# Optimization experiments

Measured on AMD Instinct MI355X. Metric: run time of the kernel, lower is better.

## Reference

```python
import jax, jax.numpy as jnp
import numpy as np

D_MODEL = 512
NHEAD = 8
WINDOW = 32  # attends to [i-32, i+32]


def setup_inputs() -> dict:
    key = jax.random.key(0)
    ks = jax.random.split(key, 5)
    B, S, D = 2, 2048, D_MODEL
    return {
        "x": jax.random.normal(ks[0], (B, S, D), dtype=jnp.float32),
        "w_qkv": jax.random.normal(ks[1], (D, 3 * D), dtype=jnp.float32) * 0.02,
        "b_qkv": jax.random.normal(ks[2], (3 * D,), dtype=jnp.float32) * 0.02,
        "w_out": jax.random.normal(ks[3], (D, D), dtype=jnp.float32) * 0.02,
        "b_out": jax.random.normal(ks[4], (D,), dtype=jnp.float32) * 0.02,
    }


def reference(x, w_qkv, b_qkv, w_out, b_out):
    B, S, D = x.shape
    H = NHEAD
    hd = D // H
    w = WINDOW
    W = 2 * w + 1

    qkv = (x @ w_qkv + b_qkv).reshape(B, S, 3, H, hd)
    q, k, v = qkv[:, :, 0], qkv[:, :, 1], qkv[:, :, 2]  # [B,S,H,hd]

    # window indices per query position: [S, W]
    idx = jnp.arange(S)[:, None] + jnp.arange(-w, w + 1)[None, :]
    valid = (idx >= 0) & (idx < S)
    idx_c = jnp.clip(idx, 0, S - 1)

    k_win = k[:, idx_c]  # [B,S,W,H,hd]
    v_win = v[:, idx_c]  # [B,S,W,H,hd]

    scale = 1.0 / (hd ** 0.5)
    scores = jnp.einsum('bshd,bswhd->bshw', q, k_win) * scale  # [B,S,H,W]
    scores = jnp.where(valid[None, :, None, :], scores, -1e9)
    attn = jax.nn.softmax(scores, axis=-1)
    out = jnp.einsum('bshw,bswhd->bshd', attn, v_win).reshape(B, S, D)
    return out @ w_out + b_out
```

## Files before the change

kernel.cpp:

```cpp
#include <hip/hip_runtime.h>


typedef __bf16 bf16x8 __attribute__((ext_vector_type(8)));
typedef float  f32x4  __attribute__((ext_vector_type(4)));
typedef unsigned short u16;
typedef unsigned int   u32;

__device__ __forceinline__ u16 f2bf(float f) {
  u32 u = __builtin_bit_cast(u32, f);
  u += 0x7FFFu + ((u >> 16) & 1u);
  return (u16)(u >> 16);
}
__device__ __forceinline__ u32 pack2(u16 a, u16 b) {
  return (u32)a | ((u32)b << 16);
}
__device__ __forceinline__ void glds16(const void* g, void* l) {
  __builtin_amdgcn_global_load_lds(
      (const __attribute__((address_space(1))) void*)g,
      (__attribute__((address_space(3))) void*)l, 16, 0, 0);
}
__device__ __forceinline__ f32x4 mfma16(bf16x8 a, bf16x8 b, f32x4 c) {
  return __builtin_amdgcn_mfma_f32_16x16x32_bf16(a, b, c, 0, 0, 0);
}

__global__ __launch_bounds__(256) void prep(
    const float4* __restrict__ X, uint2* __restrict__ XH,
    const float* __restrict__ Wq, u16* __restrict__ Wqt,
    const float* __restrict__ Wo, u16* __restrict__ Wot) {
  __shared__ float T[32][33];
  const int blk = blockIdx.x, t = threadIdx.x;
  if (blk < 2048) {
    int i = blk * 256 + t;
    float4 v = X[i];
    XH[i] = make_uint2(pack2(f2bf(v.x), f2bf(v.y)), pack2(f2bf(v.z), f2bf(v.w)));
    return;
  }
  const float* W;
  u16* Wt;
  int n0, k0, N;
  if (blk < 2816) {
    int idx = blk - 2048;
    W = Wq; Wt = Wqt; N = 1536;
    n0 = (idx % 48) * 32; k0 = (idx / 48) * 32;
  } else {
    int idx = blk - 2816;
    W = Wo; Wt = Wot; N = 512;
    n0 = (idx % 16) * 32; k0 = (idx / 16) * 32;
  }
  const int r = t >> 3, c = (t & 7) * 4;
  float4 v = *(const float4*)&W[(size_t)(k0 + r) * N + n0 + c];
  T[c][r] = v.x; T[c + 1][r] = v.y; T[c + 2][r] = v.z; T[c + 3][r] = v.w;
  __syncthreads();
  u16 a = f2bf(T[r][c]),      b = f2bf(T[r][c + 1]);
  u16 cc = f2bf(T[r][c + 2]), d = f2bf(T[r][c + 3]);
  *(uint2*)&Wt[(size_t)(n0 + r) * 512 + k0 + c] =
      make_uint2(pack2(a, b), pack2(cc, d));
}

__global__ __launch_bounds__(256) void gemm_qkv(
    const u16* __restrict__ Ah, const u16* __restrict__ Bt,
    const float* __restrict__ bias,
    u16* __restrict__ Qb, u16* __restrict__ Kb, u16* __restrict__ Vb) {
  __shared__ __align__(16) u16 sA[64 * 64];
  __shared__ __align__(16) u16 sB[128 * 64];

  const int t = threadIdx.x, l = t & 63, w = t >> 6;
  const int wm = w >> 1, wn = w & 1;
  const int mBase = blockIdx.y * 64, nBase = blockIdx.x * 128;

  const int rsub = l >> 3;
  const int qsrc = (l & 7) ^ (rsub & 7);
  const u16* gA0 = Ah + (size_t)(mBase + w * 16 + rsub) * 512 + qsrc * 8;
  const u16* gA1 = Ah + (size_t)(mBase + w * 16 + 8 + rsub) * 512 + qsrc * 8;
  u16* lA0 = sA + (w * 16) * 64;
  u16* lA1 = sA + (w * 16 + 8) * 64;
  const u16* gB[4];
  u16* lB[4];
#pragma unroll
  for (int j = 0; j < 4; ++j) {
    gB[j] = Bt + (size_t)(nBase + w * 32 + j * 8 + rsub) * 512 + qsrc * 8;
    lB[j] = sB + (w * 32 + j * 8) * 64;
  }

  const int r15 = l & 15, kg = l >> 4;
  const int sw = r15 & 7;
  int aoff[2][2], boff[4][2];
#pragma unroll
  for (int mt = 0; mt < 2; ++mt)
#pragma unroll
    for (int s = 0; s < 2; ++s)
      aoff[mt][s] = (wm * 32 + mt * 16 + r15) * 64 + (((s * 4 + kg) ^ sw) * 8);
#pragma unroll
  for (int nt = 0; nt < 4; ++nt)
#pragma unroll
    for (int s = 0; s < 2; ++s)
      boff[nt][s] = (wn * 64 + nt * 16 + r15) * 64 + (((s * 4 + kg) ^ sw) * 8);

  f32x4 acc[2][4];
#pragma unroll
  for (int i = 0; i < 2; ++i)
#pragma unroll
    for (int j = 0; j < 4; ++j) acc[i][j] = (f32x4){0.f, 0.f, 0.f, 0.f};

  for (int k0 = 0; k0 < 512; k0 += 64) {
    glds16(gA0 + k0, lA0);
    glds16(gA1 + k0, lA1);
#pragma unroll
    for (int j = 0; j < 4; ++j) glds16(gB[j] + k0, lB[j]);
    __syncthreads();
#pragma unroll
    for (int s = 0; s < 2; ++s) {
      bf16x8 b[4];
#pragma unroll
      for (int nt = 0; nt < 4; ++nt) b[nt] = *(const bf16x8*)(sB + boff[nt][s]);
      bf16x8 a0 = *(const bf16x8*)(sA + aoff[0][s]);
      bf16x8 a1 = *(const bf16x8*)(sA + aoff[1][s]);
#pragma unroll
      for (int nt = 0; nt < 4; ++nt) {
        acc[0][nt] = mfma16(a0, b[nt], acc[0][nt]);
        acc[1][nt] = mfma16(a1, b[nt], acc[1][nt]);
      }
    }
    __syncthreads();
  }

  const int lq = l >> 4;
  const int seg = nBase >> 9, colb = nBase & 511;
#pragma unroll
  for (int mt = 0; mt < 2; ++mt) {
    int row0 = mBase + wm * 32 + mt * 16 + lq * 4;
#pragma unroll
    for (int nt = 0; nt < 4; ++nt) {
      int col = wn * 64 + nt * 16 + r15;
      float bv = bias[nBase + col];
      int cc = colb + col;
      if (seg == 0) {
#pragma unroll
        for (int r = 0; r < 4; ++r)
          Qb[(size_t)(row0 + r) * 512 + cc] = f2bf((acc[mt][nt][r] + bv) * 0.125f);
      } else if (seg == 1) {
#pragma unroll
        for (int r = 0; r < 4; ++r)
          Kb[(size_t)(row0 + r) * 512 + cc] = f2bf(acc[mt][nt][r] + bv);
      } else {
#pragma unroll
        for (int r = 0; r < 4; ++r)
          Vb[(size_t)(row0 + r) * 512 + cc] = f2bf(acc[mt][nt][r] + bv);
      }
    }
  }
}

__global__ __launch_bounds__(256) void attn_mfma(
    const u16* __restrict__ Qb, const u16* __restrict__ Kb,
    const u16* __restrict__ Vb, u16* __restrict__ Oh) {
  const int tile = blockIdx.x, h = blockIdx.y, b = blockIdx.z;
  const int base = tile * 64;
  const size_t hb = (size_t)b * 2048;

  __shared__ __align__(16) u16 Qs[64][72];
  __shared__ __align__(16) u16 Ks[128][72];
  __shared__ __align__(16) u16 Vt[64][136];
  __shared__ __align__(16) u16 Pp[64][136];

  const int t = threadIdx.x, l = t & 63, w = t >> 6;
  const int r15 = l & 15, kg = l >> 4;

  {
    int r = t >> 2, c0 = (t & 3) * 16;
    const uint4* src = (const uint4*)&Qb[(hb + base + r) * 512 + h * 64 + c0];
    *(uint4*)&Qs[r][c0] = src[0];
    *(uint4*)&Qs[r][c0 + 8] = src[1];
  }
  {
    int j = t >> 1, half = (t & 1) * 32;
    int ja = min(max(base - 32 + j, 0), 2047);
    const uint4* src = (const uint4*)&Kb[(hb + ja) * 512 + h * 64 + half];
    uint4* dst = (uint4*)&Ks[j][half];
    dst[0] = src[0]; dst[1] = src[1]; dst[2] = src[2]; dst[3] = src[3];
  }
  {
    int j = t >> 1, ds = (t & 1) * 32;
    int ja = min(max(base - 32 + j, 0), 2047);
    const u16* src = &Vb[(hb + ja) * 512 + h * 64 + ds];
    u16 tmp[32];
    *(uint4*)&tmp[0]  = *(const uint4*)(src);
    *(uint4*)&tmp[8]  = *(const uint4*)(src + 8);
    *(uint4*)&tmp[16] = *(const uint4*)(src + 16);
    *(uint4*)&tmp[24] = *(const uint4*)(src + 24);
#pragma unroll
    for (int i = 0; i < 32; ++i) Vt[ds + i][j] = tmp[i];
  }
  __syncthreads();

  bf16x8 aQ0 = *(const bf16x8*)&Qs[w * 16 + r15][kg * 8];
  bf16x8 aQ1 = *(const bf16x8*)&Qs[w * 16 + r15][32 + kg * 8];
  f32x4 zero = (f32x4){0.f, 0.f, 0.f, 0.f};
  f32x4 sacc[8];
#pragma unroll
  for (int nt = 0; nt < 8; ++nt) {
    bf16x8 b0 = *(const bf16x8*)&Ks[nt * 16 + r15][kg * 8];
    bf16x8 b1 = *(const bf16x8*)&Ks[nt * 16 + r15][32 + kg * 8];
    sacc[nt] = mfma16(aQ0, b0, zero);
    sacc[nt] = mfma16(aQ1, b1, sacc[nt]);
  }

#pragma unroll
  for (int r = 0; r < 4; ++r) {
    int s_abs = base + w * 16 + kg * 4 + r;
    float m = -3.0e38f;
#pragma unroll
    for (int nt = 0; nt < 8; ++nt) {
      int j_abs = base - 32 + nt * 16 + r15;
      int dlt = j_abs - s_abs;
      bool valid = (dlt >= -32) && (dlt <= 32) && (j_abs >= 0) && (j_abs < 2048);
      float v = valid ? sacc[nt][r] : -1.0e9f;
      sacc[nt][r] = v;
      m = fmaxf(m, v);
    }
#pragma unroll
    for (int msk = 1; msk < 16; msk <<= 1) m = fmaxf(m, __shfl_xor(m, msk, 64));
    float s_ = 0.f;
#pragma unroll
    for (int nt = 0; nt < 8; ++nt) {
      float e = __expf(sacc[nt][r] - m);
      sacc[nt][r] = e;
      s_ += e;
    }
#pragma unroll
    for (int msk = 1; msk < 16; msk <<= 1) s_ += __shfl_xor(s_, msk, 64);
    float inv = 1.0f / s_;
#pragma unroll
    for (int nt = 0; nt < 8; ++nt)
      Pp[w * 16 + kg * 4 + r][nt * 16 + r15] = f2bf(sacc[nt][r] * inv);
  }
  __syncthreads();

  bf16x8 aP[4];
#pragma unroll
  for (int kt = 0; kt < 4; ++kt)
    aP[kt] = *(const bf16x8*)&Pp[w * 16 + r15][kt * 32 + kg * 8];
  f32x4 oacc[4];
#pragma unroll
  for (int nt = 0; nt < 4; ++nt) oacc[nt] = zero;
#pragma unroll
  for (int nt = 0; nt < 4; ++nt) {
#pragma unroll
    for (int kt = 0; kt < 4; ++kt) {
      bf16x8 bV = *(const bf16x8*)&Vt[nt * 16 + r15][kt * 32 + kg * 8];
      oacc[nt] = mfma16(aP[kt], bV, oacc[nt]);
    }
  }

#pragma unroll
  for (int nt = 0; nt < 4; ++nt) {
#pragma unroll
    for (int r = 0; r < 4; ++r) {
      size_t idx =
          (hb + base + w * 16 + kg * 4 + r) * 512 + h * 64 + nt * 16 + r15;
      Oh[idx] = f2bf(oacc[nt][r]);
    }
  }
}

__global__ __launch_bounds__(256) void gemm_out(
    const u16* __restrict__ Ah, const u16* __restrict__ Bt,
    const float* __restrict__ bias, float* __restrict__ Cf) {
  __shared__ __align__(16) u16 sA[64 * 64];
  __shared__ __align__(16) u16 sB[128 * 64];

  const int t = threadIdx.x, l = t & 63, w = t >> 6;
  const int wm = w >> 1, wn = w & 1;
  const int mBase = blockIdx.y * 64, nBase = blockIdx.x * 128;

  const int rsub = l >> 3;
  const int qsrc = (l & 7) ^ (rsub & 7);
  const u16* gA0 = Ah + (size_t)(mBase + w * 16 + rsub) * 512 + qsrc * 8;
  const u16* gA1 = Ah + (size_t)(mBase + w * 16 + 8 + rsub) * 512 + qsrc * 8;
  u16* lA0 = sA + (w * 16) * 64;
  u16* lA1 = sA + (w * 16 + 8) * 64;
  const u16* gB[4];
  u16* lB[4];
#pragma unroll
  for (int j = 0; j < 4; ++j) {
    gB[j] = Bt + (size_t)(nBase + w * 32 + j * 8 + rsub) * 512 + qsrc * 8;
    lB[j] = sB + (w * 32 + j * 8) * 64;
  }

  const int r15 = l & 15, kg = l >> 4;
  const int sw = r15 & 7;
  int aoff[2][2], boff[4][2];
#pragma unroll
  for (int mt = 0; mt < 2; ++mt)
#pragma unroll
    for (int s = 0; s < 2; ++s)
      aoff[mt][s] = (wm * 32 + mt * 16 + r15) * 64 + (((s * 4 + kg) ^ sw) * 8);
#pragma unroll
  for (int nt = 0; nt < 4; ++nt)
#pragma unroll
    for (int s = 0; s < 2; ++s)
      boff[nt][s] = (wn * 64 + nt * 16 + r15) * 64 + (((s * 4 + kg) ^ sw) * 8);

  f32x4 acc[2][4];
#pragma unroll
  for (int i = 0; i < 2; ++i)
#pragma unroll
    for (int j = 0; j < 4; ++j) acc[i][j] = (f32x4){0.f, 0.f, 0.f, 0.f};

  for (int k0 = 0; k0 < 512; k0 += 64) {
    glds16(gA0 + k0, lA0);
    glds16(gA1 + k0, lA1);
#pragma unroll
    for (int j = 0; j < 4; ++j) glds16(gB[j] + k0, lB[j]);
    __syncthreads();
#pragma unroll
    for (int s = 0; s < 2; ++s) {
      bf16x8 b[4];
#pragma unroll
      for (int nt = 0; nt < 4; ++nt) b[nt] = *(const bf16x8*)(sB + boff[nt][s]);
      bf16x8 a0 = *(const bf16x8*)(sA + aoff[0][s]);
      bf16x8 a1 = *(const bf16x8*)(sA + aoff[1][s]);
#pragma unroll
      for (int nt = 0; nt < 4; ++nt) {
        acc[0][nt] = mfma16(a0, b[nt], acc[0][nt]);
        acc[1][nt] = mfma16(a1, b[nt], acc[1][nt]);
      }
    }
    __syncthreads();
  }

  const int lq = l >> 4;
#pragma unroll
  for (int mt = 0; mt < 2; ++mt) {
    int row0 = mBase + wm * 32 + mt * 16 + lq * 4;
#pragma unroll
    for (int nt = 0; nt < 4; ++nt) {
      int col = nBase + wn * 64 + nt * 16 + r15;
      float bv = bias[col];
#pragma unroll
      for (int r = 0; r < 4; ++r)
        Cf[(size_t)(row0 + r) * 512 + col] = acc[mt][nt][r] + bv;
    }
  }
}

extern "C" void kernel_launch(void* const* d_in, const int* in_sizes, int n_in,
                              void* d_out, int out_size, void* d_ws, size_t ws_size,
                              hipStream_t stream) {
  const float* x     = (const float*)d_in[0];
  const float* w_qkv = (const float*)d_in[1];
  const float* b_qkv = (const float*)d_in[2];
  const float* w_out = (const float*)d_in[3];
  const float* b_out = (const float*)d_in[4];
  float* out = (float*)d_out;

  char* ws = (char*)d_ws;
  u16* xh  = (u16*)(ws + 0);
  u16* wqt = (u16*)(ws + 4194304);
  u16* wot = (u16*)(ws + 5767168);
  u16* qb  = (u16*)(ws + 6291456);
  u16* kb  = (u16*)(ws + 10485760);
  u16* vb  = (u16*)(ws + 14680064);
  u16* aoh = (u16*)(ws + 18874368);

  prep<<<3072, 256, 0, stream>>>((const float4*)x, (uint2*)xh,
                                 w_qkv, wqt, w_out, wot);
  gemm_qkv<<<dim3(12, 64), 256, 0, stream>>>(xh, wqt, b_qkv, qb, kb, vb);
  attn_mfma<<<dim3(32, 8, 2), 256, 0, stream>>>(qb, kb, vb, aoh);
  gemm_out<<<dim3(4, 64), 256, 0, stream>>>(aoh, wot, b_out, out);
}
```

Before: 101.6 us.

## Double-buffer LDS tiles in QKV and output GEMMs to overlap loads with MFMA

```diff
diff --git a/kernel.cpp b/kernel.cpp
--- a/kernel.cpp
+++ b/kernel.cpp
@@ -22,6 +22,7 @@
 __device__ __forceinline__ f32x4 mfma16(bf16x8 a, bf16x8 b, f32x4 c) {
   return __builtin_amdgcn_mfma_f32_16x16x32_bf16(a, b, c, 0, 0, 0);
 }
+#define VM0_BARRIER() asm volatile("s_waitcnt vmcnt(0)\n\ts_barrier" ::: "memory")
 
 __global__ __launch_bounds__(256) void prep(
     const float4* __restrict__ X, uint2* __restrict__ XH,
@@ -61,8 +62,8 @@
     const u16* __restrict__ Ah, const u16* __restrict__ Bt,
     const float* __restrict__ bias,
     u16* __restrict__ Qb, u16* __restrict__ Kb, u16* __restrict__ Vb) {
-  __shared__ __align__(16) u16 sA[64 * 64];
-  __shared__ __align__(16) u16 sB[128 * 64];
+  __shared__ __align__(16) u16 sA[2][64 * 64];
+  __shared__ __align__(16) u16 sB[2][128 * 64];
 
   const int t = threadIdx.x, l = t & 63, w = t >> 6;
   const int wm = w >> 1, wn = w & 1;
@@ -72,14 +73,14 @@
   const int qsrc = (l & 7) ^ (rsub & 7);
   const u16* gA0 = Ah + (size_t)(mBase + w * 16 + rsub) * 512 + qsrc * 8;
   const u16* gA1 = Ah + (size_t)(mBase + w * 16 + 8 + rsub) * 512 + qsrc * 8;
-  u16* lA0 = sA + (w * 16) * 64;
-  u16* lA1 = sA + (w * 16 + 8) * 64;
+  const int oA0 = (w * 16) * 64;
+  const int oA1 = (w * 16 + 8) * 64;
   const u16* gB[4];
-  u16* lB[4];
+  int oB[4];
 #pragma unroll
   for (int j = 0; j < 4; ++j) {
     gB[j] = Bt + (size_t)(nBase + w * 32 + j * 8 + rsub) * 512 + qsrc * 8;
-    lB[j] = sB + (w * 32 + j * 8) * 64;
+    oB[j] = (w * 32 + j * 8) * 64;
   }
 
   const int r15 = l & 15, kg = l >> 4;
@@ -102,26 +103,33 @@
 #pragma unroll
     for (int j = 0; j < 4; ++j) acc[i][j] = (f32x4){0.f, 0.f, 0.f, 0.f};
 
-  for (int k0 = 0; k0 < 512; k0 += 64) {
-    glds16(gA0 + k0, lA0);
-    glds16(gA1 + k0, lA1);
-#pragma unroll
-    for (int j = 0; j < 4; ++j) glds16(gB[j] + k0, lB[j]);
-    __syncthreads();
+  auto stage = [&](int h, int k0) {
+    glds16(gA0 + k0, sA[h] + oA0);
+    glds16(gA1 + k0, sA[h] + oA1);
+#pragma unroll
+    for (int j = 0; j < 4; ++j) glds16(gB[j] + k0, sB[h] + oB[j]);
+  };
+
+  stage(0, 0);
+#pragma unroll
+  for (int it = 0; it < 8; ++it) {
+    VM0_BARRIER();
+    if (it < 7) stage((it + 1) & 1, (it + 1) * 64);
+    const u16* sAh = sA[it & 1];
+    const u16* sBh = sB[it & 1];
 #pragma unroll
     for (int s = 0; s < 2; ++s) {
       bf16x8 b[4];
 #pragma unroll
-      for (int nt = 0; nt < 4; ++nt) b[nt] = *(const bf16x8*)(sB + boff[nt][s]);
-      bf16x8 a0 = *(const bf16x8*)(sA + aoff[0][s]);
-      bf16x8 a1 = *(const bf16x8*)(sA + aoff[1][s]);
+      for (int nt = 0; nt < 4; ++nt) b[nt] = *(const bf16x8*)(sBh + boff[nt][s]);
+      bf16x8 a0 = *(const bf16x8*)(sAh + aoff[0][s]);
+      bf16x8 a1 = *(const bf16x8*)(sAh + aoff[1][s]);
 #pragma unroll
       for (int nt = 0; nt < 4; ++nt) {
         acc[0][nt] = mfma16(a0, b[nt], acc[0][nt]);
         acc[1][nt] = mfma16(a1, b[nt], acc[1][nt]);
       }
     }
-    __syncthreads();
   }
 
   const int lq = l >> 4;
@@ -266,8 +274,8 @@
 __global__ __launch_bounds__(256) void gemm_out(
     const u16* __restrict__ Ah, const u16* __restrict__ Bt,
     const float* __restrict__ bias, float* __restrict__ Cf) {
-  __shared__ __align__(16) u16 sA[64 * 64];
-  __shared__ __align__(16) u16 sB[128 * 64];
+  __shared__ __align__(16) u16 sA[2][64 * 64];
+  __shared__ __align__(16) u16 sB[2][128 * 64];
 
   const int t = threadIdx.x, l = t & 63, w = t >> 6;
   const int wm = w >> 1, wn = w & 1;
@@ -277,14 +285,14 @@
   const int qsrc = (l & 7) ^ (rsub & 7);
   const u16* gA0 = Ah + (size_t)(mBase + w * 16 + rsub) * 512 + qsrc * 8;
   const u16* gA1 = Ah + (size_t)(mBase + w * 16 + 8 + rsub) * 512 + qsrc * 8;
-  u16* lA0 = sA + (w * 16) * 64;
-  u16* lA1 = sA + (w * 16 + 8) * 64;
+  const int oA0 = (w * 16) * 64;
+  const int oA1 = (w * 16 + 8) * 64;
   const u16* gB[4];
-  u16* lB[4];
+  int oB[4];
 #pragma unroll
   for (int j = 0; j < 4; ++j) {
     gB[j] = Bt + (size_t)(nBase + w * 32 + j * 8 + rsub) * 512 + qsrc * 8;
-    lB[j] = sB + (w * 32 + j * 8) * 64;
+    oB[j] = (w * 32 + j * 8) * 64;
   }
 
   const int r15 = l & 15, kg = l >> 4;
@@ -307,26 +315,33 @@
 #pragma unroll
     for (int j = 0; j < 4; ++j) acc[i][j] = (f32x4){0.f, 0.f, 0.f, 0.f};
 
-  for (int k0 = 0; k0 < 512; k0 += 64) {
-    glds16(gA0 + k0, lA0);
-    glds16(gA1 + k0, lA1);
-#pragma unroll
-    for (int j = 0; j < 4; ++j) glds16(gB[j] + k0, lB[j]);
-    __syncthreads();
+  auto stage = [&](int h, int k0) {
+    glds16(gA0 + k0, sA[h] + oA0);
+    glds16(gA1 + k0, sA[h] + oA1);
+#pragma unroll
+    for (int j = 0; j < 4; ++j) glds16(gB[j] + k0, sB[h] + oB[j]);
+  };
+
+  stage(0, 0);
+#pragma unroll
+  for (int it = 0; it < 8; ++it) {
+    VM0_BARRIER();
+    if (it < 7) stage((it + 1) & 1, (it + 1) * 64);
+    const u16* sAh = sA[it & 1];
+    const u16* sBh = sB[it & 1];
 #pragma unroll
     for (int s = 0; s < 2; ++s) {
       bf16x8 b[4];
 #pragma unroll
-      for (int nt = 0; nt < 4; ++nt) b[nt] = *(const bf16x8*)(sB + boff[nt][s]);
-      bf16x8 a0 = *(const bf16x8*)(sA + aoff[0][s]);
-      bf16x8 a1 = *(const bf16x8*)(sA + aoff[1][s]);
+      for (int nt = 0; nt < 4; ++nt) b[nt] = *(const bf16x8*)(sBh + boff[nt][s]);
+      bf16x8 a0 = *(const bf16x8*)(sAh + aoff[0][s]);
+      bf16x8 a1 = *(const bf16x8*)(sAh + aoff[1][s]);
 #pragma unroll
       for (int nt = 0; nt < 4; ++nt) {
         acc[0][nt] = mfma16(a0, b[nt], acc[0][nt]);
         acc[1][nt] = mfma16(a1, b[nt], acc[1][nt]);
       }
     }
-    __syncthreads();
   }
 
   const int lq = l >> 4;
```

Measured after the change: 105.4 us. +3.7%, slower.
